# Optimization experiments

Measured on AMD Instinct MI355X. Metric: run time of the kernel, lower is better.

## Reference

```python
import jax, jax.numpy as jnp
import numpy as np

D_MODEL = 1024
NUM_HEADS = 16
HEAD_DIM = D_MODEL // NUM_HEADS


def setup_inputs() -> dict:
    key = jax.random.key(0)
    ks = jax.random.split(key, 9)
    B, S = 2, 2048
    s = 1.0 / np.sqrt(D_MODEL)
    return {
        "x": jax.random.normal(ks[0], (B, S, D_MODEL), dtype=jnp.float32),
        "Wq": jax.random.normal(ks[1], (D_MODEL, D_MODEL), dtype=jnp.float32) * s,
        "bq": jnp.zeros((D_MODEL,), dtype=jnp.float32),
        "Wk": jax.random.normal(ks[2], (D_MODEL, D_MODEL), dtype=jnp.float32) * s,
        "bk": jnp.zeros((D_MODEL,), dtype=jnp.float32),
        "Wv": jax.random.normal(ks[3], (D_MODEL, D_MODEL), dtype=jnp.float32) * s,
        "bv": jnp.zeros((D_MODEL,), dtype=jnp.float32),
        "Wo": jax.random.normal(ks[4], (D_MODEL, D_MODEL), dtype=jnp.float32) * s,
        "bo": jnp.zeros((D_MODEL,), dtype=jnp.float32),
    }


def reference(x, Wq, bq, Wk, bk, Wv, bv, Wo, bo):
    B, S, _ = x.shape
    # linear projections then split heads: [B, S, D] -> [B, H, S, hd]
    def split_heads(t):
        return t.reshape(B, S, NUM_HEADS, HEAD_DIM).transpose(0, 2, 1, 3)
    q = split_heads(x @ Wq + bq)
    k = split_heads(x @ Wk + bk)
    v = split_heads(x @ Wv + bv)
    # scores: [B, H, S, S]
    scores = jnp.einsum('bhqd,bhkd->bhqk', q, k) / jnp.sqrt(
        jnp.asarray(HEAD_DIM, dtype=x.dtype))
    attn = jax.nn.softmax(scores, axis=-1)
    # dropout is identity in eval mode
    out = jnp.einsum('bhqk,bhkd->bhqd', attn, v)
    out = out.transpose(0, 2, 1, 3).reshape(B, S, D_MODEL)
    return out @ Wo + bo
```

## Files before the change

### kernel.cpp

```cpp
#include <hip/hip_runtime.h>

#define D_MODEL 1024
#define NHEAD 16
#define HD 64
#define BATCH 2
#define SEQ 2048

typedef unsigned short u16;
typedef unsigned int u32;
typedef __bf16 bf16x8 __attribute__((ext_vector_type(8)));
typedef unsigned short u16x8 __attribute__((ext_vector_type(8)));
typedef short s16x4 __attribute__((ext_vector_type(4)));
typedef float f32x4 __attribute__((ext_vector_type(4)));

static __device__ __forceinline__ u16 f2bf(float f) {
    union { float f; unsigned u; } v; v.f = f;
    unsigned u = v.u;
    u += 0x7fffu + ((u >> 16) & 1u);
    return (u16)(u >> 16);
}

static __device__ __forceinline__ void gld_lds16(const void* g, void* l) {
    __builtin_amdgcn_global_load_lds(
        (const __attribute__((address_space(1))) void*)g,
        (__attribute__((address_space(3))) void*)l, 16, 0, 0);
}

static __device__ __forceinline__ s16x4 pack_bf4(f32x4 v) {
    union { float f; unsigned u; } a, b, c, d;
    a.f = v[0]; b.f = v[1]; c.f = v[2]; d.f = v[3];
    union { unsigned u[2]; s16x4 s; } r;
    r.u[0] = __builtin_amdgcn_perm(b.u, a.u, 0x07060302u);
    r.u[1] = __builtin_amdgcn_perm(d.u, c.u, 0x07060302u);
    return r.s;
}

__global__ __launch_bounds__(256) void k_convert(const float* __restrict__ x,
                                                 const float* __restrict__ wq,
                                                 const float* __restrict__ wk,
                                                 const float* __restrict__ wv,
                                                 const float* __restrict__ wo,
                                                 u16* __restrict__ xb,
                                                 u16* __restrict__ wt) {
    int z = blockIdx.z;
    if (z == 0) {
        int base = (blockIdx.y * 32 + blockIdx.x) * 256 + threadIdx.x;
#pragma unroll
        for (int p = 0; p < 4; p++) {
            int i = base + p * 262144;
            float4 v = ((const float4*)x)[i];
            ushort4 o = make_ushort4(f2bf(v.x), f2bf(v.y), f2bf(v.z), f2bf(v.w));
            ((ushort4*)xb)[i] = o;
        }
        return;
    }
    __shared__ u16 t[32][33];
    const float* W = z == 1 ? wq : z == 2 ? wk : z == 3 ? wv : wo;
    u16* dst = wt + (size_t)(z - 1) * (D_MODEL * D_MODEL);
    int tx = threadIdx.x & 31, ty = threadIdx.x >> 5;
    int n0 = blockIdx.x * 32, k0 = blockIdx.y * 32;
#pragma unroll
    for (int i = 0; i < 4; i++)
        t[ty + i * 8][tx] = f2bf(W[(size_t)(k0 + ty + i * 8) * D_MODEL + n0 + tx]);
    __syncthreads();
#pragma unroll
    for (int i = 0; i < 4; i++)
        dst[(size_t)(n0 + ty + i * 8) * D_MODEL + k0 + tx] = t[tx][ty + i * 8];
}

__global__ __launch_bounds__(256) void k_gemm(const u16* __restrict__ A,
                                              const u16* __restrict__ WtBase,
                                              const float* __restrict__ b0,
                                              const float* __restrict__ b1,
                                              const float* __restrict__ b2,
                                              u16* __restrict__ oq, u16* __restrict__ ok,
                                              u16* __restrict__ ov) {
    __shared__ u16 lA[2 * 128 * 32];
    __shared__ u16 lB[2 * 128 * 32];
    int tid = threadIdx.x, w = tid >> 6, l = tid & 63, lr = l & 15, lq = l >> 4;
    int z = blockIdx.z;
    const u16* Wt = WtBase + (size_t)z * (D_MODEL * D_MODEL);
    const float* bias = z == 0 ? b0 : z == 1 ? b1 : b2;
    float scale = (z == 0) ? (0.125f * 1.44269504088896340736f) : 1.0f;
    int m0 = blockIdx.y * 128, n0 = blockIdx.x * 128;
    int wm = (w >> 1) * 64, wn = (w & 1) * 64;
    f32x4 acc[4][4];
#pragma unroll
    for (int mi = 0; mi < 4; mi++)
#pragma unroll
        for (int ni = 0; ni < 4; ni++) acc[mi][ni] = (f32x4){0.f, 0.f, 0.f, 0.f};

    int ra = tid >> 2, ca = (tid & 3) * 8;
    for (int kk = 0; kk < D_MODEL; kk += 64) {
#pragma unroll
        for (int kc = 0; kc < 2; kc++) {
            int cg = kk + kc * 32 + ca;
            gld_lds16(A + (size_t)(m0 + ra) * D_MODEL + cg, &lA[kc * 4096 + w * 512]);
            gld_lds16(A + (size_t)(m0 + 64 + ra) * D_MODEL + cg,
                      &lA[kc * 4096 + 2048 + w * 512]);
            gld_lds16(Wt + (size_t)(n0 + ra) * D_MODEL + cg, &lB[kc * 4096 + w * 512]);
            gld_lds16(Wt + (size_t)(n0 + 64 + ra) * D_MODEL + cg,
                      &lB[kc * 4096 + 2048 + w * 512]);
        }
        __syncthreads();
#pragma unroll
        for (int kc = 0; kc < 2; kc++) {
            bf16x8 af[4], bf[4];
#pragma unroll
            for (int mi = 0; mi < 4; mi++)
                af[mi] = *(const bf16x8*)&lA[kc * 4096 + (wm + mi * 16 + lr) * 32 + lq * 8];
#pragma unroll
            for (int ni = 0; ni < 4; ni++)
                bf[ni] = *(const bf16x8*)&lB[kc * 4096 + (wn + ni * 16 + lr) * 32 + lq * 8];
#pragma unroll
            for (int mi = 0; mi < 4; mi++)
#pragma unroll
                for (int ni = 0; ni < 4; ni++)
                    acc[mi][ni] = __builtin_amdgcn_mfma_f32_16x16x32_bf16(
                        af[mi], bf[ni], acc[mi][ni], 0, 0, 0);
        }
        __syncthreads();
    }
#pragma unroll
    for (int mi = 0; mi < 4; mi++) {
#pragma unroll
        for (int ni = 0; ni < 4; ni++) {
            int col = n0 + wn + ni * 16 + lr;
            float bval = bias[col];
            int row0 = m0 + wm + mi * 16 + lq * 4;
            if (z == 2) {
                int b = row0 >> 11, s = row0 & 2047;
                int h = col >> 6, dd = col & 63;
                ushort4 pk;
                pk.x = f2bf(acc[mi][ni][0] + bval);
                pk.y = f2bf(acc[mi][ni][1] + bval);
                pk.z = f2bf(acc[mi][ni][2] + bval);
                pk.w = f2bf(acc[mi][ni][3] + bval);
                *(ushort4*)&ov[((size_t)(b * NHEAD + h) * HD + dd) * SEQ + s] = pk;
            } else {
#pragma unroll
                for (int r = 0; r < 4; r++) {
                    int row = row0 + r;
                    float val = (acc[mi][ni][r] + bval) * scale;
                    u16* op = z == 0 ? oq : ok;
                    int b = row >> 11, s = row & 2047, h = col >> 6, d = col & 63;
                    op[(((size_t)(b * NHEAD + h)) * SEQ + s) * HD + d] = f2bf(val);
                }
            }
        }
    }
}

__global__ __launch_bounds__(256) void k_gout(const u16* __restrict__ A,
                                              const u16* __restrict__ Wt,
                                              const float* __restrict__ bias,
                                              float* __restrict__ outf) {
    __shared__ u16 lA[64 * 32];
    __shared__ u16 lB[64 * 32];
    int tid = threadIdx.x, w = tid >> 6, l = tid & 63, lr = l & 15, lq = l >> 4;
    int m0 = blockIdx.y * 64, n0 = blockIdx.x * 64;
    int wm = (w >> 1) * 32, wn = (w & 1) * 32;
    f32x4 acc[2][2];
#pragma unroll
    for (int mi = 0; mi < 2; mi++)
#pragma unroll
        for (int ni = 0; ni < 2; ni++) acc[mi][ni] = (f32x4){0.f, 0.f, 0.f, 0.f};

    int ra = tid >> 2, ca = (tid & 3) * 8;
    for (int kk = 0; kk < D_MODEL; kk += 32) {
        gld_lds16(A + (size_t)(m0 + ra) * D_MODEL + kk + ca, &lA[w * 512]);
        gld_lds16(Wt + (size_t)(n0 + ra) * D_MODEL + kk + ca, &lB[w * 512]);
        __syncthreads();
        bf16x8 af[2], bf[2];
#pragma unroll
        for (int mi = 0; mi < 2; mi++)
            af[mi] = *(const bf16x8*)&lA[(wm + mi * 16 + lr) * 32 + lq * 8];
#pragma unroll
        for (int ni = 0; ni < 2; ni++)
            bf[ni] = *(const bf16x8*)&lB[(wn + ni * 16 + lr) * 32 + lq * 8];
#pragma unroll
        for (int mi = 0; mi < 2; mi++)
#pragma unroll
            for (int ni = 0; ni < 2; ni++)
                acc[mi][ni] = __builtin_amdgcn_mfma_f32_16x16x32_bf16(
                    af[mi], bf[ni], acc[mi][ni], 0, 0, 0);
        __syncthreads();
    }
#pragma unroll
    for (int mi = 0; mi < 2; mi++)
#pragma unroll
        for (int ni = 0; ni < 2; ni++) {
            int col = n0 + wn + ni * 16 + lr;
            float bval = bias[col];
#pragma unroll
            for (int r = 0; r < 4; r++) {
                int row = m0 + wm + mi * 16 + lq * 4 + r;
                outf[(size_t)row * D_MODEL + col] = acc[mi][ni][r] + bval;
            }
        }
}

__global__ __launch_bounds__(256) void k_attn(const u16* __restrict__ Q,
                                              const u16* __restrict__ K,
                                              const u16* __restrict__ VT,
                                              u16* __restrict__ part0,
                                              u16* __restrict__ part1,
                                              float* __restrict__ lsum, int nsplit) {
    __shared__ u16 lK[128 * 72];
    __shared__ u16 lVt[64 * 136];
    int tid = threadIdx.x, w = tid >> 6, l = tid & 63, lr = l & 15, lq = l >> 4;
    int bl = blockIdx.x;
    int qt = bl / (32 * nsplit);
    int rem = bl - qt * (32 * nsplit);
    int bh = rem / nsplit;
    int ks = rem - bh * nsplit;
    int qb = qt * 128 + w * 32;
    const u16* Qb = Q + (size_t)bh * SEQ * HD;
    const u16* Kb = K + (size_t)bh * SEQ * HD;
    const u16* VTb = VT + (size_t)bh * HD * SEQ;

    bf16x8 qf[2][2];
#pragma unroll
    for (int tq = 0; tq < 2; tq++)
#pragma unroll
        for (int kc = 0; kc < 2; kc++)
            qf[tq][kc] = *(const bf16x8*)&Qb[(size_t)(qb + tq * 16 + lr) * HD +
                                             kc * 32 + lq * 8];
    f32x4 o[2][4];
    f32x4 ol[2];
#pragma unroll
    for (int tq = 0; tq < 2; tq++) {
        ol[tq] = (f32x4){0.f, 0.f, 0.f, 0.f};
#pragma unroll
        for (int di = 0; di < 4; di++) o[tq][di] = (f32x4){0.f, 0.f, 0.f, 0.f};
    }
    const s16x4 vones = {(short)0x3F80, (short)0x3F80, (short)0x3F80, (short)0x3F80};

    int krow = tid >> 3, kch = tid & 7;
    int vrow = tid >> 4, vch = tid & 15;

    int nk = SEQ / nsplit;
    int jbeg = ks * nk, jend = jbeg + nk;

    u16x8 kreg[4], vreg[4];
#pragma unroll
    for (int p = 0; p < 4; p++) {
        kreg[p] = *(const u16x8*)&Kb[(size_t)(jbeg + p * 32 + krow) * HD + kch * 8];
        vreg[p] = *(const u16x8*)&VTb[(size_t)(p * 16 + vrow) * SEQ + jbeg + vch * 8];
    }

    for (int j0 = jbeg; j0 < jend; j0 += 128) {
        __syncthreads();
#pragma unroll
        for (int p = 0; p < 4; p++) {
            *(u16x8*)&lK[(p * 32 + krow) * 72 + kch * 8] = kreg[p];
            *(u16x8*)&lVt[(p * 16 + vrow) * 136 + vch * 8] = vreg[p];
        }
        __syncthreads();
        if (j0 + 128 < jend) {
            int jn = j0 + 128;
#pragma unroll
            for (int p = 0; p < 4; p++) {
                kreg[p] = *(const u16x8*)&Kb[(size_t)(jn + p * 32 + krow) * HD + kch * 8];
                vreg[p] = *(const u16x8*)&VTb[(size_t)(p * 16 + vrow) * SEQ + jn + vch * 8];
            }
        }

#pragma unroll
        for (int kh = 0; kh < 2; kh++) {
#pragma unroll
            for (int tk = 0; tk < 4; tk++) {
                int row = kh * 64 + tk * 16 + lr;
                bf16x8 kf0 = *(const bf16x8*)&lK[row * 72 + lq * 8];
                bf16x8 kf1 = *(const bf16x8*)&lK[row * 72 + 32 + lq * 8];
                f32x4 s0 = (f32x4){0.f, 0.f, 0.f, 0.f};
                f32x4 s1 = (f32x4){0.f, 0.f, 0.f, 0.f};
                s0 = __builtin_amdgcn_mfma_f32_16x16x32_bf16(kf0, qf[0][0], s0, 0, 0, 0);
                s0 = __builtin_amdgcn_mfma_f32_16x16x32_bf16(kf1, qf[0][1], s0, 0, 0, 0);
                s1 = __builtin_amdgcn_mfma_f32_16x16x32_bf16(kf0, qf[1][0], s1, 0, 0, 0);
                s1 = __builtin_amdgcn_mfma_f32_16x16x32_bf16(kf1, qf[1][1], s1, 0, 0, 0);
#pragma unroll
                for (int r = 0; r < 4; r++) {
                    s0[r] = exp2f(s0[r]);
                    s1[r] = exp2f(s1[r]);
                }
                s16x4 pf0 = pack_bf4(s0);
                s16x4 pf1 = pack_bf4(s1);
                ol[0] = __builtin_amdgcn_mfma_f32_16x16x16bf16_1k(
                    pf0, vones, ol[0], 0, 0, 0);
                ol[1] = __builtin_amdgcn_mfma_f32_16x16x16bf16_1k(
                    pf1, vones, ol[1], 0, 0, 0);
#pragma unroll
                for (int di = 0; di < 4; di++) {
                    s16x4 vf = *(const s16x4*)&lVt[(di * 16 + lr) * 136 +
                                                   kh * 64 + tk * 16 + lq * 4];
                    o[0][di] = __builtin_amdgcn_mfma_f32_16x16x16bf16_1k(
                        pf0, vf, o[0][di], 0, 0, 0);
                    o[1][di] = __builtin_amdgcn_mfma_f32_16x16x16bf16_1k(
                        pf1, vf, o[1][di], 0, 0, 0);
                }
            }
        }
    }
    int b = bh >> 4, h = bh & 15;
    if (nsplit == 1) {
#pragma unroll
        for (int tq = 0; tq < 2; tq++) {
#pragma unroll
            for (int di = 0; di < 4; di++)
#pragma unroll
                for (int r = 0; r < 4; r++) {
                    int qg = qb + tq * 16 + lq * 4 + r;
                    part0[((size_t)(b * SEQ + qg)) * D_MODEL + h * 64 + di * 16 + lr] =
                        f2bf(o[tq][di][r] / ol[tq][r]);
                }
        }
    } else {
        u16* pdst = (ks == 0) ? part0 : part1;
#pragma unroll
        for (int tq = 0; tq < 2; tq++)
#pragma unroll
            for (int di = 0; di < 4; di++)
#pragma unroll
                for (int r = 0; r < 4; r++) {
                    int qg = qb + tq * 16 + lq * 4 + r;
                    union { _Float16 h; u16 u; } cv;
                    cv.h = (_Float16)o[tq][di][r];
                    pdst[((size_t)(b * SEQ + qg)) * D_MODEL + h * 64 + di * 16 + lr] =
                        cv.u;
                }
        if (lr == 0) {
#pragma unroll
            for (int tq = 0; tq < 2; tq++)
#pragma unroll
                for (int r = 0; r < 4; r++) {
                    int qg = qb + tq * 16 + lq * 4 + r;
                    lsum[(ks * 32 + bh) * 2048 + qg] = ol[tq][r];
                }
        }
    }
}

__global__ __launch_bounds__(256) void k_combine(const u16* __restrict__ p0,
                                                 const u16* __restrict__ p1,
                                                 const float* __restrict__ lsum,
                                                 u16* __restrict__ dst) {
    int i = blockIdx.x * 256 + threadIdx.x;
    size_t a8 = (size_t)i * 8;
    int row = (int)(a8 >> 10);
    int col = (int)(a8 & 1023);
    int b = row >> 11, q = row & 2047, h = col >> 6;
    int mi = ((b << 4) + h) * 2048 + q;
    float inv = 1.0f / (lsum[mi] + lsum[65536 + mi]);
    u16x8 h0 = *(const u16x8*)(p0 + a8);
    u16x8 h1 = *(const u16x8*)(p1 + a8);
    u16x8 out;
#pragma unroll
    for (int j = 0; j < 8; j++) {
        union { _Float16 h; u16 u; } c0, c1;
        c0.u = h0[j]; c1.u = h1[j];
        out[j] = f2bf(((float)c0.h + (float)c1.h) * inv);
    }
    *(u16x8*)(dst + a8) = out;
}

extern "C" void kernel_launch(void* const* d_in, const int* in_sizes, int n_in,
                              void* d_out, int out_size, void* d_ws, size_t ws_size,
                              hipStream_t stream) {
    const float* x  = (const float*)d_in[0];
    const float* Wq = (const float*)d_in[1];
    const float* bq = (const float*)d_in[2];
    const float* Wk = (const float*)d_in[3];
    const float* bk = (const float*)d_in[4];
    const float* Wv = (const float*)d_in[5];
    const float* bv = (const float*)d_in[6];
    const float* Wo = (const float*)d_in[7];
    const float* bo = (const float*)d_in[8];
    float* out = (float*)d_out;

    char* ws = (char*)d_ws;
    u16* xb  = (u16*)ws;
    u16* wt  = (u16*)(ws + (size_t)8 * 1024 * 1024);
    u16* qws = (u16*)(ws + (size_t)16 * 1024 * 1024);
    u16* kws = (u16*)(ws + (size_t)24 * 1024 * 1024);
    u16* vtw = (u16*)(ws + (size_t)32 * 1024 * 1024);
    u16* ao  = (u16*)(ws + (size_t)40 * 1024 * 1024);
    float* ml = (float*)(ws + (size_t)48 * 1024 * 1024);

    int nsplit = (ws_size >= (size_t)49 * 1024 * 1024) ? 2 : 1;
    u16* attn_out = (nsplit == 2) ? xb : ao;

    k_convert<<<dim3(32, 32, 5), 256, 0, stream>>>(x, Wq, Wk, Wv, Wo, xb, wt);
    k_gemm<<<dim3(8, 32, 3), 256, 0, stream>>>(xb, wt, bq, bk, bv, qws, kws, vtw);
    if (nsplit == 2) {
        k_attn<<<16 * 32 * 2, 256, 0, stream>>>(qws, kws, vtw, xb, ao, ml, 2);
        k_combine<<<2048, 256, 0, stream>>>(xb, ao, ml, xb);
    } else {
        k_attn<<<16 * 32, 256, 0, stream>>>(qws, kws, vtw, ao, nullptr, ml, 1);
    }
    k_gout<<<dim3(16, 64), 256, 0, stream>>>(attn_out,
                                             wt + (size_t)3 * D_MODEL * D_MODEL,
                                             bo, out);
}
```

Before: 228.0 us.

## Use 16x16x32 MFMA for PV, swizzle LDS tiles, add setprio and fast exp2

The attention inner loop now handles two 16-key tiles at once, so the P·V and row-sum products use the K=32 bf16 MFMA instead of pairs of K=16 MFMAs. Both halves of the P fragment are packed into one 8-wide vector. The padded LDS layouts for K and V^T are replaced by XOR-swizzled unpadded layouts to avoid bank conflicts and cut LDS use. It also wraps the MFMA blocks in s_setprio and switches exp2f to the hardware exp2 builtin, which skips the library's range handling.

```diff
diff --git a/kernel.cpp b/kernel.cpp
--- a/kernel.cpp
+++ b/kernel.cpp
@@ -13,6 +13,16 @@
 typedef short s16x4 __attribute__((ext_vector_type(4)));
 typedef float f32x4 __attribute__((ext_vector_type(4)));
 
+#if defined(__has_builtin)
+#if __has_builtin(__builtin_amdgcn_exp2f)
+#define EXP2(x) __builtin_amdgcn_exp2f(x)
+#else
+#define EXP2(x) exp2f(x)
+#endif
+#else
+#define EXP2(x) exp2f(x)
+#endif
+
 static __device__ __forceinline__ u16 f2bf(float f) {
     union { float f; unsigned u; } v; v.f = f;
     unsigned u = v.u;
@@ -26,13 +36,16 @@
         (__attribute__((address_space(3))) void*)l, 16, 0, 0);
 }
 
-static __device__ __forceinline__ s16x4 pack_bf4(f32x4 v) {
-    union { float f; unsigned u; } a, b, c, d;
-    a.f = v[0]; b.f = v[1]; c.f = v[2]; d.f = v[3];
-    union { unsigned u[2]; s16x4 s; } r;
-    r.u[0] = __builtin_amdgcn_perm(b.u, a.u, 0x07060302u);
-    r.u[1] = __builtin_amdgcn_perm(d.u, c.u, 0x07060302u);
-    return r.s;
+static __device__ __forceinline__ bf16x8 pack_bf8(f32x4 a, f32x4 b) {
+    union { float f; unsigned u; } a0, a1, a2, a3, b0, b1, b2, b3;
+    a0.f = a[0]; a1.f = a[1]; a2.f = a[2]; a3.f = a[3];
+    b0.f = b[0]; b1.f = b[1]; b2.f = b[2]; b3.f = b[3];
+    union { unsigned u[4]; bf16x8 v; } r;
+    r.u[0] = __builtin_amdgcn_perm(a1.u, a0.u, 0x07060302u);
+    r.u[1] = __builtin_amdgcn_perm(a3.u, a2.u, 0x07060302u);
+    r.u[2] = __builtin_amdgcn_perm(b1.u, b0.u, 0x07060302u);
+    r.u[3] = __builtin_amdgcn_perm(b3.u, b2.u, 0x07060302u);
+    return r.v;
 }
 
 __global__ __launch_bounds__(256) void k_convert(const float* __restrict__ x,
@@ -200,14 +213,21 @@
         }
 }
 
+static __device__ __forceinline__ int ksw(int row, int col) {
+    return row * 64 + ((((col >> 3) ^ (row & 7)) << 3) | (col & 7));
+}
+static __device__ __forceinline__ int vsw(int row, int col) {
+    return row * 128 + ((((col >> 3) ^ (row & 15)) << 3) | (col & 7));
+}
+
 __global__ __launch_bounds__(256) void k_attn(const u16* __restrict__ Q,
                                               const u16* __restrict__ K,
                                               const u16* __restrict__ VT,
                                               u16* __restrict__ part0,
                                               u16* __restrict__ part1,
                                               float* __restrict__ lsum, int nsplit) {
-    __shared__ u16 lK[128 * 72];
-    __shared__ u16 lVt[64 * 136];
+    __shared__ __align__(16) u16 lK[128 * 64];
+    __shared__ __align__(16) u16 lVt[64 * 128];
     int tid = threadIdx.x, w = tid >> 6, l = tid & 63, lr = l & 15, lq = l >> 4;
     int bl = blockIdx.x;
     int qt = bl / (32 * nsplit);
@@ -234,7 +254,10 @@
 #pragma unroll
         for (int di = 0; di < 4; di++) o[tq][di] = (f32x4){0.f, 0.f, 0.f, 0.f};
     }
-    const s16x4 vones = {(short)0x3F80, (short)0x3F80, (short)0x3F80, (short)0x3F80};
+    union { u16 s[8]; bf16x8 v; } onev;
+#pragma unroll
+    for (int i = 0; i < 8; i++) onev.s[i] = 0x3F80;
+    const bf16x8 vone8 = onev.v;
 
     int krow = tid >> 3, kch = tid & 7;
     int vrow = tid >> 4, vch = tid & 15;
@@ -253,8 +276,8 @@
         __syncthreads();
 #pragma unroll
         for (int p = 0; p < 4; p++) {
-            *(u16x8*)&lK[(p * 32 + krow) * 72 + kch * 8] = kreg[p];
-            *(u16x8*)&lVt[(p * 16 + vrow) * 136 + vch * 8] = vreg[p];
+            *(u16x8*)&lK[ksw(p * 32 + krow, kch * 8)] = kreg[p];
+            *(u16x8*)&lVt[vsw(p * 16 + vrow, vch * 8)] = vreg[p];
         }
         __syncthreads();
         if (j0 + 128 < jend) {
@@ -269,36 +292,51 @@
 #pragma unroll
         for (int kh = 0; kh < 2; kh++) {
 #pragma unroll
-            for (int tk = 0; tk < 4; tk++) {
-                int row = kh * 64 + tk * 16 + lr;
-                bf16x8 kf0 = *(const bf16x8*)&lK[row * 72 + lq * 8];
-                bf16x8 kf1 = *(const bf16x8*)&lK[row * 72 + 32 + lq * 8];
-                f32x4 s0 = (f32x4){0.f, 0.f, 0.f, 0.f};
-                f32x4 s1 = (f32x4){0.f, 0.f, 0.f, 0.f};
-                s0 = __builtin_amdgcn_mfma_f32_16x16x32_bf16(kf0, qf[0][0], s0, 0, 0, 0);
-                s0 = __builtin_amdgcn_mfma_f32_16x16x32_bf16(kf1, qf[0][1], s0, 0, 0, 0);
-                s1 = __builtin_amdgcn_mfma_f32_16x16x32_bf16(kf0, qf[1][0], s1, 0, 0, 0);
-                s1 = __builtin_amdgcn_mfma_f32_16x16x32_bf16(kf1, qf[1][1], s1, 0, 0, 0);
+            for (int t2 = 0; t2 < 2; t2++) {
+                int rA = kh * 64 + t2 * 32 + lr;
+                int rB = rA + 16;
+                bf16x8 kA0 = *(const bf16x8*)&lK[ksw(rA, lq * 8)];
+                bf16x8 kA1 = *(const bf16x8*)&lK[ksw(rA, 32 + lq * 8)];
+                bf16x8 kB0 = *(const bf16x8*)&lK[ksw(rB, lq * 8)];
+                bf16x8 kB1 = *(const bf16x8*)&lK[ksw(rB, 32 + lq * 8)];
+                f32x4 sA0 = (f32x4){0.f, 0.f, 0.f, 0.f};
+                f32x4 sA1 = (f32x4){0.f, 0.f, 0.f, 0.f};
+                f32x4 sB0 = (f32x4){0.f, 0.f, 0.f, 0.f};
+                f32x4 sB1 = (f32x4){0.f, 0.f, 0.f, 0.f};
+                __builtin_amdgcn_s_setprio(1);
+                sA0 = __builtin_amdgcn_mfma_f32_16x16x32_bf16(kA0, qf[0][0], sA0, 0, 0, 0);
+                sB0 = __builtin_amdgcn_mfma_f32_16x16x32_bf16(kB0, qf[0][0], sB0, 0, 0, 0);
+                sA1 = __builtin_amdgcn_mfma_f32_16x16x32_bf16(kA0, qf[1][0], sA1, 0, 0, 0);
+                sB1 = __builtin_amdgcn_mfma_f32_16x16x32_bf16(kB0, qf[1][0], sB1, 0, 0, 0);
+                sA0 = __builtin_amdgcn_mfma_f32_16x16x32_bf16(kA1, qf[0][1], sA0, 0, 0, 0);
+                sB0 = __builtin_amdgcn_mfma_f32_16x16x32_bf16(kB1, qf[0][1], sB0, 0, 0, 0);
+                sA1 = __builtin_amdgcn_mfma_f32_16x16x32_bf16(kA1, qf[1][1], sA1, 0, 0, 0);
+                sB1 = __builtin_amdgcn_mfma_f32_16x16x32_bf16(kB1, qf[1][1], sB1, 0, 0, 0);
+                __builtin_amdgcn_s_setprio(0);
 #pragma unroll
                 for (int r = 0; r < 4; r++) {
-                    s0[r] = exp2f(s0[r]);
-                    s1[r] = exp2f(s1[r]);
-                }
-                s16x4 pf0 = pack_bf4(s0);
-                s16x4 pf1 = pack_bf4(s1);
-                ol[0] = __builtin_amdgcn_mfma_f32_16x16x16bf16_1k(
-                    pf0, vones, ol[0], 0, 0, 0);
-                ol[1] = __builtin_amdgcn_mfma_f32_16x16x16bf16_1k(
-                    pf1, vones, ol[1], 0, 0, 0);
+                    sA0[r] = EXP2(sA0[r]);
+                    sA1[r] = EXP2(sA1[r]);
+                    sB0[r] = EXP2(sB0[r]);
+                    sB1[r] = EXP2(sB1[r]);
+                }
+                bf16x8 pf0 = pack_bf8(sA0, sB0);
+                bf16x8 pf1 = pack_bf8(sA1, sB1);
+                __builtin_amdgcn_s_setprio(1);
+                ol[0] = __builtin_amdgcn_mfma_f32_16x16x32_bf16(pf0, vone8, ol[0], 0, 0, 0);
+                ol[1] = __builtin_amdgcn_mfma_f32_16x16x32_bf16(pf1, vone8, ol[1], 0, 0, 0);
 #pragma unroll
                 for (int di = 0; di < 4; di++) {
-                    s16x4 vf = *(const s16x4*)&lVt[(di * 16 + lr) * 136 +
-                                                   kh * 64 + tk * 16 + lq * 4];
-                    o[0][di] = __builtin_amdgcn_mfma_f32_16x16x16bf16_1k(
-                        pf0, vf, o[0][di], 0, 0, 0);
-                    o[1][di] = __builtin_amdgcn_mfma_f32_16x16x16bf16_1k(
-                        pf1, vf, o[1][di], 0, 0, 0);
-                }
+                    int vr = di * 16 + lr;
+                    union { bf16x8 v; s16x4 h[2]; } vv;
+                    vv.h[0] = *(const s16x4*)&lVt[vsw(vr, kh * 64 + t2 * 32 + lq * 4)];
+                    vv.h[1] = *(const s16x4*)&lVt[vsw(vr, kh * 64 + t2 * 32 + 16 + lq * 4)];
+                    o[0][di] = __builtin_amdgcn_mfma_f32_16x16x32_bf16(pf0, vv.v,
+                                                                       o[0][di], 0, 0, 0);
+                    o[1][di] = __builtin_amdgcn_mfma_f32_16x16x32_bf16(pf1, vv.v,
+                                                                       o[1][di], 0, 0, 0);
+                }
+                __builtin_amdgcn_s_setprio(0);
             }
         }
     }
```

Result: faster. 205.7 us (-9.8%).
